# Optimization experiments

Hardware: AMD Instinct MI355X
Metric: run time of the kernel (lower is better)

The kernel has to match this reference:

```python
import jax, jax.numpy as jnp
import numpy as np

B, T, C = 4, 2048, 768
H = 12
D = C // H  # head dim 64

def setup_inputs() -> dict:
    key = jax.random.key(0)
    ks = jax.random.split(key, 6)
    scale = 1.0 / np.sqrt(C)
    x = jax.random.normal(ks[0], (B, T, C), dtype=jnp.float32)
    attention_mask = jax.random.randint(ks[1], (B, T), 0, 2, dtype=jnp.int64)
    Wqkv = jax.random.normal(ks[2], (C, 3 * C), dtype=jnp.float32) * scale
    bqkv = jax.random.normal(ks[3], (3 * C,), dtype=jnp.float32) * 0.02
    Wo = jax.random.normal(ks[4], (C, C), dtype=jnp.float32) * scale
    bo = jax.random.normal(ks[5], (C,), dtype=jnp.float32) * 0.02
    return {"x": x, "attention_mask": attention_mask, "Wqkv": Wqkv,
            "bqkv": bqkv, "Wo": Wo, "bo": bo}

def reference(x, attention_mask, Wqkv, bqkv, Wo, bo):
    # fused QKV projection: [B,T,3C]
    qkv = jnp.einsum('btc,cd->btd', x, Wqkv) + bqkv
    q, k, v = jnp.split(qkv, 3, axis=-1)
    # reshape to [B,H,T,D]
    q = q.reshape(B, T, H, D).transpose(0, 2, 1, 3)
    k = k.reshape(B, T, H, D).transpose(0, 2, 1, 3)
    v = v.reshape(B, T, H, D).transpose(0, 2, 1, 3)
    # module quirk: True (attended) where attention_mask == 0
    keep = (attention_mask == 0)[:, None, None, :]  # [B,1,1,T]
    scores = jnp.einsum('bhqd,bhkd->bhqk', q, k) / np.sqrt(D)
    scores = jnp.where(keep, scores, jnp.finfo(scores.dtype).min)
    probs = jax.nn.softmax(scores, axis=-1)
    context = jnp.einsum('bhqk,bhkd->bhqd', probs, v)
    context = context.transpose(0, 2, 1, 3).reshape(B, T, C)
    return jnp.einsum('btc,cd->btd', context, Wo) + bo
```

## Files before the change

### kernel.cpp

```cpp
#include <hip/hip_runtime.h>
#include <stdint.h>

#define AS1 __attribute__((address_space(1)))
#define AS3 __attribute__((address_space(3)))

typedef _Float16 f16;
typedef _Float16 f16x8 __attribute__((ext_vector_type(8)));
typedef _Float16 f16x4 __attribute__((ext_vector_type(4)));
typedef float    f32x4  __attribute__((ext_vector_type(4)));
typedef float    f32x16 __attribute__((ext_vector_type(16)));
typedef uint32_t u32x4  __attribute__((ext_vector_type(4)));
typedef uint32_t u32x2  __attribute__((ext_vector_type(2)));

#define B_  4
#define T_  2048
#define C_  768
#define H_  12
#define D_  64
#define M_  (B_*T_)
#define N1_ (3*C_)

__device__ __forceinline__ void g2l16(const void* g, void* l) {
  __builtin_amdgcn_global_load_lds((const AS1 void*)g, (AS3 void*)l, 16, 0, 0);
}

__device__ __forceinline__ f32x4 fzero4() { f32x4 z = {0.f, 0.f, 0.f, 0.f}; return z; }

__device__ __forceinline__ uint32_t pk_u32(float a, float b) {
  auto t = __builtin_amdgcn_cvt_pkrtz(a, b);
  return *(uint32_t*)&t;
}

__device__ __forceinline__ void pl32swap(uint32_t& d, uint32_t& s) {
  u32x2 r = __builtin_amdgcn_permlane32_swap(d, s, false, false);
  d = r[0]; s = r[1];
}

__global__ __launch_bounds__(256)
void prep_kernel(const float* __restrict__ Wqkv, f16* __restrict__ WqkvT,
                 const float* __restrict__ Wo, f16* __restrict__ WoT,
                 const float* __restrict__ x, f16* __restrict__ xh,
                 int* __restrict__ idx, int* __restrict__ cnt) {
  __shared__ float tile[32][33];
  const int blk = blockIdx.x;
  if (blk < 2304) {
    const float* in; f16* out; int R, C, bx, by;
    if (blk < 1728) { in = Wqkv; out = WqkvT; R = 768; C = 2304; bx = blk % 72; by = blk / 72; }
    else { const int k = blk - 1728; in = Wo; out = WoT; R = 768; C = 768; bx = k % 24; by = k / 24; }
    const int tx = threadIdx.x & 31, ty = threadIdx.x >> 5;
    const int c0 = bx * 32, r0 = by * 32;
#pragma unroll
    for (int i = 0; i < 32; i += 8)
      tile[ty + i][tx] = in[(long)(r0 + ty + i) * C + c0 + tx];
    __syncthreads();
#pragma unroll
    for (int i = 0; i < 32; i += 8)
      out[(long)(c0 + ty + i) * R + r0 + tx] = (f16)tile[tx][ty + i];
  } else if (blk < 8448) {
    const int i = ((blk - 2304) * 256 + threadIdx.x) * 4;
    const float4 v = *(const float4*)(x + i);
    f16x4 o = {(f16)v.x, (f16)v.y, (f16)v.z, (f16)v.w};
    *(f16x4*)(xh + i) = o;
  } else {
    const int g = (blk - 8448) * 256 + threadIdx.x;
    idx[g] = 0;
    if (g < B_) cnt[g] = 0;
  }
}

__global__ __launch_bounds__(256)
void compact_kernel(const int* __restrict__ mask, int* __restrict__ idx,
                    int* __restrict__ cnt) {
  const int b = blockIdx.y;
  const int t = blockIdx.x * 256 + threadIdx.x;
  if (mask[b * T_ + t] == 0) {
    const int s = atomicAdd(&cnt[b], 1);
    idx[b * T_ + s] = t;
  }
}

template <typename OutT>
__global__ __launch_bounds__(256)
void gemm_bias_kernel(const f16* __restrict__ A, const f16* __restrict__ Bt,
                      const float* __restrict__ bias, OutT* __restrict__ Cc,
                      int K, int ldc) {
  __shared__ f16 lA[2 * 128 * 32];
  __shared__ f16 lB[2 * 128 * 32];
  const int tid = threadIdx.x;
  const int n0 = blockIdx.x * 128, m0 = blockIdx.y * 128;
  const int lane = tid & 63, w = tid >> 6;
  const int wm = (w & 1) * 64, wn = (w >> 1) * 64;
  const int r15 = lane & 15, q4 = lane >> 4;
  const int rkey = (r15 >> 1) & 3;

  const int r0 = tid >> 2, jj = tid & 3;
  const int scol = (jj ^ ((r0 >> 1) & 3)) * 8;
  const f16* pA0 = A + (long)(m0 + r0) * K + scol;
  const f16* pB0 = Bt + (long)(n0 + r0) * K + scol;
  const long rstep = (long)64 * K;

  f32x4 acc[4][4];
#pragma unroll
  for (int i = 0; i < 4; i++)
#pragma unroll
    for (int j = 0; j < 4; j++) acc[i][j] = fzero4();

#define STAGE_WO(bufsel, kb) do {                                   \
  const int lb = (bufsel) * 4096;                                   \
  g2l16(pA0 + (kb), &lA[lb + tid * 8]);                             \
  g2l16(pA0 + rstep + (kb), &lA[lb + 2048 + tid * 8]);              \
  g2l16(pB0 + (kb), &lB[lb + tid * 8]);                             \
  g2l16(pB0 + rstep + (kb), &lB[lb + 2048 + tid * 8]);              \
} while (0)

#define COMPUTE_WO(bufsel) do {                                     \
  const int lb = (bufsel) * 4096;                                   \
  const int cofs = (q4 ^ rkey) * 8;                                 \
  f16x8 af[4], bfv[4];                                              \
  _Pragma("unroll")                                                 \
  for (int mi = 0; mi < 4; mi++)                                    \
    af[mi] = *(const f16x8*)&lA[lb + (wm + mi * 16 + r15) * 32 + cofs]; \
  _Pragma("unroll")                                                 \
  for (int ni = 0; ni < 4; ni++)                                    \
    bfv[ni] = *(const f16x8*)&lB[lb + (wn + ni * 16 + r15) * 32 + cofs]; \
  _Pragma("unroll")                                                 \
  for (int mi = 0; mi < 4; mi++)                                    \
    _Pragma("unroll")                                               \
    for (int ni = 0; ni < 4; ni++)                                  \
      acc[mi][ni] = __builtin_amdgcn_mfma_f32_16x16x32_f16(af[mi], bfv[ni], acc[mi][ni], 0, 0, 0); \
} while (0)

  STAGE_WO(0, 0);
  __syncthreads();

  int cur = 0;
  const int NT = K / 32;
  for (int t = 0; t < NT - 1; t++) {
    STAGE_WO(cur ^ 1, (t + 1) * 32);
    COMPUTE_WO(cur);
    __syncthreads();
    cur ^= 1;
  }
  COMPUTE_WO(cur);

#undef STAGE_WO
#undef COMPUTE_WO

#pragma unroll
  for (int ni = 0; ni < 4; ni++) {
    const int col = n0 + wn + ni * 16 + r15;
    const float bs = bias[col];
#pragma unroll
    for (int mi = 0; mi < 4; mi++) {
#pragma unroll
      for (int r = 0; r < 4; r++) {
        const int row = m0 + wm + mi * 16 + q4 * 4 + r;
        Cc[(long)row * ldc + col] = (OutT)(acc[mi][ni][r] + bs);
      }
    }
  }
}

__global__ __launch_bounds__(512, 2)
void gemm_qkv256(const f16* __restrict__ A, const f16* __restrict__ Bt,
                 const float* __restrict__ bias, f16* __restrict__ Qb,
                 f16* __restrict__ Kc, f16* __restrict__ Vt,
                 const int* __restrict__ idx, const int* __restrict__ cnt) {
  const int K = C_;
  __shared__ f16 lA[2 * 256 * 64];
  __shared__ f16 lB[2 * 256 * 64];
  const int tid = threadIdx.x;
  const int nb = blockIdx.x;
  const int mb = blockIdx.y;
  const bool isQ = nb < 3;

  int b = 0, s0 = 0;
  if (!isQ) {
    b = mb >> 3;
    s0 = (mb & 7) * 256;
    if (s0 >= cnt[b]) return;
  }

  const int lane = tid & 63, w = tid >> 6;
  const int wmi = w >> 2, wni = w & 3;
  const int r15 = lane & 15, q4 = lane >> 4;
  const int rx = (r15 & 7) * 8;

  const int trow = tid >> 3;
  const int koffsw = (((tid & 7) ^ (trow & 7)) * 8);
  const f16* pA[4];
  const f16* pB[4];
#pragma unroll
  for (int i = 0; i < 4; i++) {
    const int ri = i * 64 + trow;
    long grow;
    if (isQ) grow = (long)mb * 256 + ri;
    else     grow = (long)b * T_ + idx[b * T_ + s0 + ri];
    pA[i] = A + grow * K + koffsw;
    pB[i] = Bt + (long)(nb * 256 + ri) * K + koffsw;
  }
  const int lofs = tid * 8;

  f32x4 acc[8][4];
#pragma unroll
  for (int i = 0; i < 8; i++)
#pragma unroll
    for (int j = 0; j < 4; j++) acc[i][j] = fzero4();

#define STAGE_QKV(bufsel, kb) do {                                        \
  const int lb = (bufsel) * 16384;                                        \
  _Pragma("unroll")                                                       \
  for (int i = 0; i < 4; i++) {                                           \
    g2l16(pA[i] + (kb), &lA[lb + i * 4096 + lofs]);                       \
    g2l16(pB[i] + (kb), &lB[lb + i * 4096 + lofs]);                       \
  }                                                                       \
} while (0)

#define COMPUTE_QKV(bufsel) do {                                          \
  const int lb = (bufsel) * 16384;                                        \
  _Pragma("unroll")                                                       \
  for (int kh = 0; kh < 2; kh++) {                                        \
    const int cofs = (kh * 32 + q4 * 8) ^ rx;                             \
    f16x8 af[8], bf[4];                                                   \
    _Pragma("unroll")                                                     \
    for (int mi = 0; mi < 8; mi++)                                        \
      af[mi] = *(const f16x8*)&lA[lb + (wmi * 128 + mi * 16 + r15) * 64 + cofs]; \
    _Pragma("unroll")                                                     \
    for (int ni = 0; ni < 4; ni++)                                        \
      bf[ni] = *(const f16x8*)&lB[lb + (wni * 64 + ni * 16 + r15) * 64 + cofs];  \
    _Pragma("unroll")                                                     \
    for (int mi = 0; mi < 8; mi++)                                        \
      _Pragma("unroll")                                                   \
      for (int ni = 0; ni < 4; ni++)                                      \
        acc[mi][ni] = __builtin_amdgcn_mfma_f32_16x16x32_f16(af[mi], bf[ni], acc[mi][ni], 0, 0, 0); \
  }                                                                       \
} while (0)

  STAGE_QKV(0, 0);
  __syncthreads();

  int cur = 0;
  const int NT = K / 64;
  for (int t = 0; t < NT - 1; t++) {
    STAGE_QKV(cur ^ 1, (t + 1) * 64);
    COMPUTE_QKV(cur);
    __syncthreads();
    cur ^= 1;
  }
  COMPUTE_QKV(cur);

#undef STAGE_QKV
#undef COMPUTE_QKV

#pragma unroll
  for (int ni = 0; ni < 4; ni++) {
    const int cN = nb * 256 + wni * 64 + ni * 16 + r15;
    const float bs = bias[cN];
    if (isQ) {
#pragma unroll
      for (int mi = 0; mi < 8; mi++)
#pragma unroll
        for (int r = 0; r < 4; r++) {
          const long row = (long)mb * 256 + wmi * 128 + mi * 16 + q4 * 4 + r;
          Qb[row * C_ + cN] = (f16)(acc[mi][ni][r] + bs);
        }
    } else if (cN < 2 * C_) {
      const int ocol = cN - C_;
#pragma unroll
      for (int mi = 0; mi < 8; mi++)
#pragma unroll
        for (int r = 0; r < 4; r++) {
          const long row = (long)b * T_ + s0 + wmi * 128 + mi * 16 + q4 * 4 + r;
          Kc[row * C_ + ocol] = (f16)(acc[mi][ni][r] + bs);
        }
    } else {
      const int vcol = cN - 2 * C_;
      const int vh = vcol >> 6, d = vcol & 63;
      f16* dst = Vt + ((long)(b * H_ + vh) * D_ + d) * T_;
#pragma unroll
      for (int mi = 0; mi < 8; mi++) {
        const long slot = s0 + wmi * 128 + mi * 16 + q4 * 4;
        f16x4 v4;
#pragma unroll
        for (int r = 0; r < 4; r++) v4[r] = (f16)(acc[mi][ni][r] + bs);
        *(f16x4*)&dst[slot] = v4;
      }
    }
  }
}

__global__ __launch_bounds__(256, 4)
void attn_kernel(const f16* __restrict__ Qb, const f16* __restrict__ Kc,
                 const f16* __restrict__ vtc, const int* __restrict__ cnt,
                 f16* __restrict__ ctx) {
  __shared__ f16 Ks[2][64 * 64];
  __shared__ f16 Vs[2][64 * 64];
  __shared__ float Ls[4][32];
  const int tid = threadIdx.x, lane = tid & 63, w = tid >> 6;
  const int l31 = lane & 31, hh = lane >> 5;

  const int g = blockIdx.y * 16 + blockIdx.x;
  const int xcd = g & 7, local = g >> 3;
  const int bh = xcd * 6 + (local >> 4);
  const int q0 = (local & 15) * 128;
  const int b = bh / H_, h = bh % H_;

  const f16* Qg = Qb + (long)(b * T_ + q0) * C_ + h * D_;
  const f16* Kbase = Kc + (long)b * T_ * C_ + h * D_;
  const f16* Vg = vtc + (long)bh * D_ * T_;
  const int nk = cnt[b];
  const int nkt = (nk + 63) >> 6;

  const f16 qsc = (f16)0.18033688f;
  f16x8 bq[4];
#pragma unroll
  for (int j = 0; j < 4; j++) {
    f16x8 v = *(const f16x8*)(Qg + (long)(w * 32 + l31) * C_ + j * 16 + hh * 8);
#pragma unroll
    for (int e = 0; e < 8; e++) v[e] = v[e] * qsc;
    bq[j] = v;
  }

  const int r_0 = w * 16 + (lane >> 3);
  const int sc = ((lane & 7) ^ (r_0 & 7)) * 8;
  const f16* Ksrc0 = Kbase + (long)r_0 * C_ + sc;
  const f16* Ksrc1 = Kbase + (long)(r_0 + 8) * C_ + sc;
  const f16* Vsrc0 = Vg + (long)r_0 * T_ + sc;
  const f16* Vsrc1 = Vg + (long)(r_0 + 8) * T_ + sc;
  const int ld0 = w * 1024 + lane * 8;
  const int ld1 = ld0 + 512;

#define ATTN_STAGE(bs, kt) do {                                  \
    g2l16(Ksrc0 + (long)(kt) * C_, &Ks[bs][ld0]);                \
    g2l16(Ksrc1 + (long)(kt) * C_, &Ks[bs][ld1]);                \
    g2l16(Vsrc0 + (kt), &Vs[bs][ld0]);                           \
    g2l16(Vsrc1 + (kt), &Vs[bs][ld1]);                           \
  } while (0)

  float l_acc = 0.f;
  f32x16 O[2];
#pragma unroll
  for (int dt = 0; dt < 2; dt++)
#pragma unroll
    for (int r = 0; r < 16; r++) O[dt][r] = 0.f;

  const int swz = l31 & 7;

  ATTN_STAGE(0, 0);
  __syncthreads();

  int cur = 0;
  for (int t = 0; t < nkt; t++) {
    const int kt = t * 64;
    if (t + 1 < nkt) ATTN_STAGE(cur ^ 1, kt + 64);

    u32x4 paw[4];
    const bool full = (kt + 64 <= nk);
#pragma unroll
    for (int t2 = 0; t2 < 2; t2++) {
      f32x16 acc;
      if (full) {
#pragma unroll
        for (int r = 0; r < 16; r++) acc[r] = 0.f;
      } else {
        const int kbase = kt + t2 * 32 + hh * 4;
#pragma unroll
        for (int g4 = 0; g4 < 4; g4++)
#pragma unroll
          for (int i = 0; i < 4; i++)
            acc[4 * g4 + i] = (kbase + 8 * g4 + i < nk) ? 0.f : -1e30f;
      }
      __builtin_amdgcn_s_setprio(1);
#pragma unroll
      for (int j = 0; j < 4; j++) {
        f16x8 ak = *(const f16x8*)&Ks[cur][(t2 * 32 + l31) * 64 + (((j * 2 + hh) ^ swz) << 3)];
        acc = __builtin_amdgcn_mfma_f32_32x32x16_f16(ak, bq[j], acc, 0, 0, 0);
      }
      __builtin_amdgcn_s_setprio(0);
      uint32_t wg[4], xg[4];
#pragma unroll
      for (int g4 = 0; g4 < 4; g4++) {
        const float p0 = __builtin_amdgcn_exp2f(acc[4 * g4 + 0]);
        const float p1 = __builtin_amdgcn_exp2f(acc[4 * g4 + 1]);
        const float p2 = __builtin_amdgcn_exp2f(acc[4 * g4 + 2]);
        const float p3 = __builtin_amdgcn_exp2f(acc[4 * g4 + 3]);
        l_acc += (p0 + p1) + (p2 + p3);
        wg[g4] = pk_u32(p0, p1);
        xg[g4] = pk_u32(p2, p3);
      }
#pragma unroll
      for (int jl = 0; jl < 2; jl++) {
        uint32_t w0 = wg[2 * jl], w2v = wg[2 * jl + 1];
        uint32_t w1 = xg[2 * jl], w3v = xg[2 * jl + 1];
        pl32swap(w0, w2v);
        pl32swap(w1, w3v);
        paw[2 * t2 + jl][0] = w0;  paw[2 * t2 + jl][1] = w1;
        paw[2 * t2 + jl][2] = w2v; paw[2 * t2 + jl][3] = w3v;
      }
    }

    __builtin_amdgcn_s_setprio(1);
#pragma unroll
    for (int j = 0; j < 4; j++) {
      const f16x8 pa = *(const f16x8*)&paw[j];
#pragma unroll
      for (int dt = 0; dt < 2; dt++) {
        const int vrow = dt * 32 + l31;
        f16x8 vb = *(const f16x8*)&Vs[cur][vrow * 64 + (((j * 2 + hh) ^ swz) << 3)];
        O[dt] = __builtin_amdgcn_mfma_f32_32x32x16_f16(pa, vb, O[dt], 0, 0, 0);
      }
    }
    __builtin_amdgcn_s_setprio(0);

    __syncthreads();
    cur ^= 1;
  }
#undef ATTN_STAGE

  l_acc += __shfl_xor(l_acc, 32);
  asm volatile("s_waitcnt lgkmcnt(0)" ::: "memory");
  if (hh == 0) Ls[w][l31] = l_acc;
  asm volatile("s_waitcnt lgkmcnt(0)" ::: "memory");
#pragma unroll
  for (int g4 = 0; g4 < 4; g4++) {
    const f32x4 lv = *(const f32x4*)&Ls[w][g4 * 8 + hh * 4];
#pragma unroll
    for (int i = 0; i < 4; i++) {
      const float inv = 1.f / lv[i];
      const int row = b * T_ + q0 + w * 32 + g4 * 8 + hh * 4 + i;
#pragma unroll
      for (int dt = 0; dt < 2; dt++)
        ctx[(long)row * C_ + h * D_ + dt * 32 + l31] = (f16)(O[dt][4 * g4 + i] * inv);
    }
  }
}

extern "C" void kernel_launch(void* const* d_in, const int* in_sizes, int n_in,
                              void* d_out, int out_size, void* d_ws, size_t ws_size,
                              hipStream_t stream) {
  (void)in_sizes; (void)n_in; (void)out_size; (void)ws_size;
  const float* x    = (const float*)d_in[0];
  const int*   mask = (const int*)  d_in[1];
  const float* Wqkv = (const float*)d_in[2];
  const float* bqkv = (const float*)d_in[3];
  const float* Wo   = (const float*)d_in[4];
  const float* bo   = (const float*)d_in[5];
  float* out = (float*)d_out;

  char* ws = (char*)d_ws;
  const size_t OFF_WQKVT = 0;
  const size_t OFF_WOT   = OFF_WQKVT + 3538944;
  const size_t OFF_Q     = OFF_WOT + 1179648;
  const size_t OFF_KC    = OFF_Q + 12582912;
  const size_t OFF_VT    = OFF_KC + 12582912;
  const size_t OFF_XH    = OFF_VT + 12582912;
  const size_t OFF_IDX   = OFF_XH + 12582912;
  const size_t OFF_CNT   = OFF_IDX + 32768;
  f16* WqkvT = (f16*)(ws + OFF_WQKVT);
  f16* WoT   = (f16*)(ws + OFF_WOT);
  f16* Qb    = (f16*)(ws + OFF_Q);
  f16* Kc    = (f16*)(ws + OFF_KC);
  f16* Vtc   = (f16*)(ws + OFF_VT);
  f16* xh    = (f16*)(ws + OFF_XH);
  f16* ctx   = (f16*)(ws + OFF_XH);
  int* idx   = (int*)(ws + OFF_IDX);
  int* cnt   = (int*)(ws + OFF_CNT);

  prep_kernel<<<dim3(8480), 256, 0, stream>>>(Wqkv, WqkvT, Wo, WoT, x, xh, idx, cnt);
  compact_kernel<<<dim3(T_ / 256, B_), 256, 0, stream>>>(mask, idx, cnt);
  gemm_qkv256<<<dim3(9, 32), 512, 0, stream>>>(xh, WqkvT, bqkv, Qb, Kc, Vtc, idx, cnt);
  attn_kernel<<<dim3(16, 48), 256, 0, stream>>>(Qb, Kc, Vtc, cnt, ctx);
  gemm_bias_kernel<float><<<dim3(6, 64), 256, 0, stream>>>(ctx, WoT, bo, out, 768, 768);
}
```

Before: 187.9 us.

## Restructure QKV GEMM into 4-stage K=32 pipeline with interleaved loads

The QKV projection GEMM mainloop changes from a double-buffered K=64 tile to a 4-deep ring of K=32 tiles. A and B loads are issued three stages ahead and split across the two compute halves, with manual vmcnt waits and raw s_barrier in place of __syncthreads. MFMA blocks are wrapped in s_setprio and the LDS swizzle is adapted to 32-wide rows. The goal is to hide global load latency and cut barrier stalls. The cost is twice as many barriers per K and fragile hand-tuned waitcnt accounting.

Result: no change. 190.8 us (+1.5%).

```diff
diff --git a/kernel.cpp b/kernel.cpp
--- a/kernel.cpp
+++ b/kernel.cpp
@@ -167,8 +167,8 @@
                  f16* __restrict__ Kc, f16* __restrict__ Vt,
                  const int* __restrict__ idx, const int* __restrict__ cnt) {
   const int K = C_;
-  __shared__ f16 lA[2 * 256 * 64];
-  __shared__ f16 lB[2 * 256 * 64];
+  __shared__ f16 lA[4 * 256 * 32];
+  __shared__ f16 lB[4 * 256 * 32];
   const int tid = threadIdx.x;
   const int nb = blockIdx.x;
   const int mb = blockIdx.y;
@@ -184,22 +184,20 @@
   const int lane = tid & 63, w = tid >> 6;
   const int wmi = w >> 2, wni = w & 3;
   const int r15 = lane & 15, q4 = lane >> 4;
-  const int rx = (r15 & 7) * 8;
-
-  const int trow = tid >> 3;
-  const int koffsw = (((tid & 7) ^ (trow & 7)) * 8);
-  const f16* pA[4];
-  const f16* pB[4];
-#pragma unroll
-  for (int i = 0; i < 4; i++) {
-    const int ri = i * 64 + trow;
-    long grow;
-    if (isQ) grow = (long)mb * 256 + ri;
-    else     grow = (long)b * T_ + idx[b * T_ + s0 + ri];
-    pA[i] = A + grow * K + koffsw;
-    pB[i] = Bt + (long)(nb * 256 + ri) * K + koffsw;
-  }
-  const int lofs = tid * 8;
+  const int cofs = ((q4 ^ ((r15 >> 1) & 3)) * 8);
+
+  const int trow = tid >> 2, jj = tid & 3;
+  const int scol = (jj ^ ((trow >> 1) & 3)) * 8;
+  long grow0, grow1;
+  if (isQ) { grow0 = (long)mb * 256 + trow; grow1 = grow0 + 128; }
+  else {
+    grow0 = (long)b * T_ + idx[b * T_ + s0 + trow];
+    grow1 = (long)b * T_ + idx[b * T_ + s0 + trow + 128];
+  }
+  const f16* pA0 = A + grow0 * K + scol;
+  const f16* pA1 = A + grow1 * K + scol;
+  const f16* pB0 = Bt + (long)(nb * 256 + trow) * K + scol;
+  const f16* pB1 = pB0 + (long)128 * K;
 
   f32x4 acc[8][4];
 #pragma unroll
@@ -207,50 +205,67 @@
 #pragma unroll
     for (int j = 0; j < 4; j++) acc[i][j] = fzero4();
 
-#define STAGE_QKV(bufsel, kb) do {                                        \
-  const int lb = (bufsel) * 16384;                                        \
-  _Pragma("unroll")                                                       \
-  for (int i = 0; i < 4; i++) {                                           \
-    g2l16(pA[i] + (kb), &lA[lb + i * 4096 + lofs]);                       \
-    g2l16(pB[i] + (kb), &lB[lb + i * 4096 + lofs]);                       \
-  }                                                                       \
-} while (0)
-
-#define COMPUTE_QKV(bufsel) do {                                          \
-  const int lb = (bufsel) * 16384;                                        \
-  _Pragma("unroll")                                                       \
-  for (int kh = 0; kh < 2; kh++) {                                        \
-    const int cofs = (kh * 32 + q4 * 8) ^ rx;                             \
-    f16x8 af[8], bf[4];                                                   \
-    _Pragma("unroll")                                                     \
-    for (int mi = 0; mi < 8; mi++)                                        \
-      af[mi] = *(const f16x8*)&lA[lb + (wmi * 128 + mi * 16 + r15) * 64 + cofs]; \
-    _Pragma("unroll")                                                     \
-    for (int ni = 0; ni < 4; ni++)                                        \
-      bf[ni] = *(const f16x8*)&lB[lb + (wni * 64 + ni * 16 + r15) * 64 + cofs];  \
-    _Pragma("unroll")                                                     \
-    for (int mi = 0; mi < 8; mi++)                                        \
-      _Pragma("unroll")                                                   \
-      for (int ni = 0; ni < 4; ni++)                                      \
-        acc[mi][ni] = __builtin_amdgcn_mfma_f32_16x16x32_f16(af[mi], bf[ni], acc[mi][ni], 0, 0, 0); \
-  }                                                                       \
-} while (0)
-
-  STAGE_QKV(0, 0);
-  __syncthreads();
-
-  int cur = 0;
-  const int NT = K / 64;
-  for (int t = 0; t < NT - 1; t++) {
-    STAGE_QKV(cur ^ 1, (t + 1) * 64);
-    COMPUTE_QKV(cur);
-    __syncthreads();
-    cur ^= 1;
-  }
-  COMPUTE_QKV(cur);
-
-#undef STAGE_QKV
-#undef COMPUTE_QKV
+#define STAGE_A_(bufsel, kb) do {                                   \
+    g2l16(pA0 + (kb), &lA[(bufsel) * 8192 + tid * 8]);              \
+    g2l16(pA1 + (kb), &lA[(bufsel) * 8192 + 4096 + tid * 8]);       \
+  } while (0)
+#define STAGE_B_(bufsel, kb) do {                                   \
+    g2l16(pB0 + (kb), &lB[(bufsel) * 8192 + tid * 8]);              \
+    g2l16(pB1 + (kb), &lB[(bufsel) * 8192 + 4096 + tid * 8]);       \
+  } while (0)
+
+  STAGE_A_(0, 0);  STAGE_B_(0, 0);
+  STAGE_A_(1, 32); STAGE_B_(1, 32);
+  STAGE_A_(2, 64); STAGE_B_(2, 64);
+  asm volatile("s_waitcnt vmcnt(8)" ::: "memory");
+  __builtin_amdgcn_s_barrier();
+  asm volatile("" ::: "memory");
+
+  const int NT = K / 32;
+  for (int t = 0; t < NT; t++) {
+    const int lb = (t & 3) * 8192;
+    f16x8 bf[4];
+    if (t < NT - 3) STAGE_A_((t + 3) & 3, (t + 3) * 32);
+    {
+      f16x8 af[4];
+#pragma unroll
+      for (int mi = 0; mi < 4; mi++)
+        af[mi] = *(const f16x8*)&lA[lb + (wmi * 128 + mi * 16 + r15) * 32 + cofs];
+#pragma unroll
+      for (int ni = 0; ni < 4; ni++)
+        bf[ni] = *(const f16x8*)&lB[lb + (wni * 64 + ni * 16 + r15) * 32 + cofs];
+      __builtin_amdgcn_s_setprio(1);
+#pragma unroll
+      for (int mi = 0; mi < 4; mi++)
+#pragma unroll
+        for (int ni = 0; ni < 4; ni++)
+          acc[mi][ni] = __builtin_amdgcn_mfma_f32_16x16x32_f16(af[mi], bf[ni], acc[mi][ni], 0, 0, 0);
+      __builtin_amdgcn_s_setprio(0);
+    }
+    if (t < NT - 3) STAGE_B_((t + 3) & 3, (t + 3) * 32);
+    {
+      f16x8 af[4];
+#pragma unroll
+      for (int mi = 0; mi < 4; mi++)
+        af[mi] = *(const f16x8*)&lA[lb + (wmi * 128 + (mi + 4) * 16 + r15) * 32 + cofs];
+      __builtin_amdgcn_s_setprio(1);
+#pragma unroll
+      for (int mi = 0; mi < 4; mi++)
+#pragma unroll
+        for (int ni = 0; ni < 4; ni++)
+          acc[mi + 4][ni] = __builtin_amdgcn_mfma_f32_16x16x32_f16(af[mi], bf[ni], acc[mi + 4][ni], 0, 0, 0);
+      __builtin_amdgcn_s_setprio(0);
+    }
+    if (t < NT - 3) { asm volatile("s_waitcnt vmcnt(8)" ::: "memory"); }
+    else if (t == NT - 3) { asm volatile("s_waitcnt vmcnt(4)" ::: "memory"); }
+    else if (t == NT - 2) { asm volatile("s_waitcnt vmcnt(0)" ::: "memory"); }
+    if (t < NT - 1) {
+      __builtin_amdgcn_s_barrier();
+      asm volatile("" ::: "memory");
+    }
+  }
+#undef STAGE_A_
+#undef STAGE_B_
 
 #pragma unroll
   for (int ni = 0; ni < 4; ni++) {
```
